# Optimization experiments

Measured on AMD Instinct MI355X. Metric: run time of the kernel, lower is better.

## Reference

```python
import jax, jax.numpy as jnp
import numpy as np

NNZ = 524288
IN_FEATURES = 50000
OUT_FEATURES = 512
N_ROWS = 4096


def setup_inputs() -> dict:
    key = jax.random.key(0)
    k1, k2, k3, k4, k5 = jax.random.split(key, 5)
    values = jax.random.normal(k1, (NNZ,), dtype=jnp.float32)
    weight = jax.random.normal(k2, (IN_FEATURES, OUT_FEATURES), dtype=jnp.float32)
    bias = jax.random.normal(k3, (OUT_FEATURES,), dtype=jnp.float32)
    rows = jax.random.randint(k4, (NNZ,), 0, N_ROWS)
    cols = jax.random.randint(k5, (NNZ,), 0, IN_FEATURES)
    return {
        "values": values,
        "weight": weight,
        "bias": bias,
        "rows": rows,
        "cols": cols,
        "n_rows": N_ROWS,
    }


def reference(values, weight, bias, rows, cols, n_rows):
    # SpMM: out[r, :] = sum_{k: rows[k]==r} values[k] * weight[cols[k], :]
    contrib = values[:, None] * weight[cols]               # [nnz, out]
    out = jax.ops.segment_sum(contrib, rows, num_segments=n_rows)  # [n_rows, out]
    return out + bias
```

## Files before the change

kernel.cpp:

```cpp
#include <hip/hip_runtime.h>
#include <hip/hip_fp16.h>


typedef float f4v __attribute__((ext_vector_type(4)));
typedef int   i4v __attribute__((ext_vector_type(4)));
typedef int   i2v __attribute__((ext_vector_type(2)));

__global__ void convert_count_kernel(const float* __restrict__ weight,
                                     __half* __restrict__ wf16, long long ngroups16,
                                     const int* __restrict__ rows,
                                     int* __restrict__ counts, int nnz) {
    long long i = (long long)blockIdx.x * blockDim.x + threadIdx.x;

    int nquads = nnz >> 2;
    if (i < nquads) {
        i4v r = ((const i4v*)rows)[i];
        atomicAdd(&counts[r.x], 1);
        atomicAdd(&counts[r.y], 1);
        atomicAdd(&counts[r.z], 1);
        atomicAdd(&counts[r.w], 1);
    } else if (i == nquads) {
        for (int k = nquads * 4; k < nnz; ++k) atomicAdd(&counts[rows[k]], 1);
    }

    const f4v* w4 = (const f4v*)weight;
    f4v* dst = (f4v*)wf16;
    long long stride = (long long)gridDim.x * blockDim.x;
    for (long long g = i; g < ngroups16; g += stride) {
        f4v a = w4[4 * g + 0];
        f4v b = w4[4 * g + 1];
        f4v c = w4[4 * g + 2];
        f4v d = w4[4 * g + 3];
        union { __half2 h2[4]; f4v v; } u0, u1;
        u0.h2[0] = __floats2half2_rn(a.x, a.y);
        u0.h2[1] = __floats2half2_rn(a.z, a.w);
        u0.h2[2] = __floats2half2_rn(b.x, b.y);
        u0.h2[3] = __floats2half2_rn(b.z, b.w);
        u1.h2[0] = __floats2half2_rn(c.x, c.y);
        u1.h2[1] = __floats2half2_rn(c.z, c.w);
        u1.h2[2] = __floats2half2_rn(d.x, d.y);
        u1.h2[3] = __floats2half2_rn(d.z, d.w);
        __builtin_nontemporal_store(u0.v, &dst[2 * g]);
        __builtin_nontemporal_store(u1.v, &dst[2 * g + 1]);
    }
}

__global__ void scan_kernel(const int* __restrict__ counts, int* __restrict__ offsets,
                            int* __restrict__ cursor, int n_rows) {
    __shared__ int partial[256];
    const int t = threadIdx.x;
    const int per = (n_rows + 255) / 256;
    const int base = t * per;
    const bool vec = (base + per <= n_rows) && ((per & 3) == 0);

    int sum = 0;
    if (vec) {
        const i4v* c4 = (const i4v*)(counts + base);
        for (int j = 0; j < per / 4; ++j) {
            i4v q = c4[j];
            sum += q.x + q.y + q.z + q.w;
        }
    } else {
        for (int j = 0; j < per; ++j) {
            int idx = base + j;
            if (idx < n_rows) sum += counts[idx];
        }
    }
    partial[t] = sum;
    __syncthreads();
    for (int off = 1; off < 256; off <<= 1) {
        int v = 0;
        if (t >= off) v = partial[t - off];
        __syncthreads();
        if (t >= off) partial[t] += v;
        __syncthreads();
    }
    int run = (t == 0) ? 0 : partial[t - 1];
    if (vec) {
        const i4v* c4 = (const i4v*)(counts + base);
        i4v* o4 = (i4v*)(offsets + base);
        i4v* u4 = (i4v*)(cursor + base);
        for (int j = 0; j < per / 4; ++j) {
            i4v q = c4[j];
            i4v o;
            o.x = run; run += q.x;
            o.y = run; run += q.y;
            o.z = run; run += q.z;
            o.w = run; run += q.w;
            o4[j] = o;
            u4[j] = o;
        }
    } else {
        for (int j = 0; j < per; ++j) {
            int idx = base + j;
            if (idx < n_rows) {
                offsets[idx] = run;
                cursor[idx] = run;
                run += counts[idx];
            }
        }
    }
    if (t == 255) offsets[n_rows] = run;
}

__global__ void scatter_pairs_kernel(const int* __restrict__ rows, const int* __restrict__ cols,
                                     const float* __restrict__ values, int* __restrict__ cursor,
                                     int2* __restrict__ pairs, int nnz) {
    int i = blockIdx.x * blockDim.x + threadIdx.x;
    int nquads = nnz >> 2;
    if (i < nquads) {
        i4v r = ((const i4v*)rows)[i];
        i4v c = ((const i4v*)cols)[i];
        f4v v = ((const f4v*)values)[i];
        int p0 = atomicAdd(&cursor[r.x], 1);
        pairs[p0] = make_int2(c.x, __float_as_int(v.x));
        int p1 = atomicAdd(&cursor[r.y], 1);
        pairs[p1] = make_int2(c.y, __float_as_int(v.y));
        int p2 = atomicAdd(&cursor[r.z], 1);
        pairs[p2] = make_int2(c.z, __float_as_int(v.z));
        int p3 = atomicAdd(&cursor[r.w], 1);
        pairs[p3] = make_int2(c.w, __float_as_int(v.w));
    } else if (i == nquads) {
        for (int k = nquads * 4; k < nnz; ++k) {
            int p = atomicAdd(&cursor[rows[k]], 1);
            pairs[p] = make_int2(cols[k], __float_as_int(values[k]));
        }
    }
}

__global__ __launch_bounds__(256) void accum_f16_kernel(
    const __half* __restrict__ wf16, const float* __restrict__ bias,
    const int* __restrict__ offsets, const int2* __restrict__ pairs,
    float* __restrict__ out, int out_f) {
    const int wave = threadIdx.x >> 6;
    const int lane = threadIdx.x & 63;
    const int row = blockIdx.x;
    const int start = offsets[row];
    const int end = offsets[row + 1];
    const int len = end - start;
    const int per = (len + 3) >> 2;
    int p = start + wave * per;
    int pe = p + per;
    if (pe > end) pe = end;
    if (p > end) p = end;

    const f4v* wbase = (const f4v*)wf16;
    const i2v* pbase = (const i2v*)pairs;
    float acc[8] = {0.f, 0.f, 0.f, 0.f, 0.f, 0.f, 0.f, 0.f};

    for (; p + 4 <= pe; p += 4) {
        i2v e0 = __builtin_nontemporal_load(pbase + p);
        i2v e1 = __builtin_nontemporal_load(pbase + p + 1);
        i2v e2 = __builtin_nontemporal_load(pbase + p + 2);
        i2v e3 = __builtin_nontemporal_load(pbase + p + 3);
        f4v w0 = wbase[(long long)e0.x * 64 + lane];
        f4v w1 = wbase[(long long)e1.x * 64 + lane];
        f4v w2 = wbase[(long long)e2.x * 64 + lane];
        f4v w3 = wbase[(long long)e3.x * 64 + lane];
        float v0 = __int_as_float(e0.y);
        float v1 = __int_as_float(e1.y);
        float v2 = __int_as_float(e2.y);
        float v3 = __int_as_float(e3.y);
        const __half2* h0 = (const __half2*)&w0;
        const __half2* h1 = (const __half2*)&w1;
        const __half2* h2 = (const __half2*)&w2;
        const __half2* h3 = (const __half2*)&w3;
#pragma unroll
        for (int j = 0; j < 4; ++j) {
            float2 f0 = __half22float2(h0[j]);
            float2 f1 = __half22float2(h1[j]);
            float2 f2 = __half22float2(h2[j]);
            float2 f3 = __half22float2(h3[j]);
            acc[2 * j]     += v0 * f0.x + v1 * f1.x + v2 * f2.x + v3 * f3.x;
            acc[2 * j + 1] += v0 * f0.y + v1 * f1.y + v2 * f2.y + v3 * f3.y;
        }
    }
    for (; p < pe; ++p) {
        i2v e0 = __builtin_nontemporal_load(pbase + p);
        float v0 = __int_as_float(e0.y);
        f4v w0 = wbase[(long long)e0.x * 64 + lane];
        const __half2* h0 = (const __half2*)&w0;
#pragma unroll
        for (int j = 0; j < 4; ++j) {
            float2 f0 = __half22float2(h0[j]);
            acc[2 * j]     += v0 * f0.x;
            acc[2 * j + 1] += v0 * f0.y;
        }
    }

    __shared__ float red[4][512];
    {
        float4* dstp = (float4*)&red[wave][lane * 8];
        dstp[0] = make_float4(acc[0], acc[1], acc[2], acc[3]);
        dstp[1] = make_float4(acc[4], acc[5], acc[6], acc[7]);
    }
    __syncthreads();
    const int c = threadIdx.x * 2;
    float s0 = red[0][c] + red[1][c] + red[2][c] + red[3][c];
    float s1 = red[0][c + 1] + red[1][c + 1] + red[2][c + 1] + red[3][c + 1];
    float2 b = *(const float2*)(bias + c);
    *(float2*)(out + (long long)row * out_f + c) = make_float2(s0 + b.x, s1 + b.y);
}

__global__ void count_rows_kernel(const int* __restrict__ rows, int* __restrict__ counts, int nnz) {
    int i = blockIdx.x * blockDim.x + threadIdx.x;
    if (i < nnz) atomicAdd(&counts[rows[i]], 1);
}
__global__ void scatter_kernel(const int* __restrict__ rows, int* __restrict__ cursor,
                               int* __restrict__ perm, int nnz) {
    int i = blockIdx.x * blockDim.x + threadIdx.x;
    if (i < nnz) {
        int p = atomicAdd(&cursor[rows[i]], 1);
        perm[p] = i;
    }
}
__global__ void accum_kernel(const float* __restrict__ values, const float* __restrict__ weight,
                             const float* __restrict__ bias, const int* __restrict__ cols,
                             const int* __restrict__ offsets, const int* __restrict__ perm,
                             float* __restrict__ out, int out_f) {
    const int r = blockIdx.x;
    const int start = offsets[r];
    const int end = offsets[r + 1];
    const int step = blockDim.x * 4;
    for (int base = threadIdx.x * 4; base < out_f; base += step) {
        float4 acc = make_float4(0.f, 0.f, 0.f, 0.f);
        for (int p = start; p < end; ++p) {
            int k = perm[p];
            float v = values[k];
            long long c = cols[k];
            float4 w = *(const float4*)(weight + c * (long long)out_f + base);
            acc.x += v * w.x; acc.y += v * w.y; acc.z += v * w.z; acc.w += v * w.w;
        }
        float4 b = *(const float4*)(bias + base);
        acc.x += b.x; acc.y += b.y; acc.z += b.z; acc.w += b.w;
        *(float4*)(out + (long long)r * out_f + base) = acc;
    }
}

static size_t align_up(size_t x, size_t a) { return (x + a - 1) & ~(a - 1); }

extern "C" void kernel_launch(void* const* d_in, const int* in_sizes, int n_in,
                              void* d_out, int out_size, void* d_ws, size_t ws_size,
                              hipStream_t stream) {
    const float* values = (const float*)d_in[0];
    const float* weight = (const float*)d_in[1];
    const float* bias   = (const float*)d_in[2];
    const int*   rows   = (const int*)d_in[3];
    const int*   cols   = (const int*)d_in[4];

    const int nnz = in_sizes[0];
    const long long wtotal = in_sizes[1];
    const int out_f = in_sizes[2];
    const int n_rows = out_size / out_f;
    float* out = (float*)d_out;

    size_t off_wf16 = 0;
    size_t off_counts = align_up(off_wf16 + (size_t)wtotal * sizeof(__half), 256);
    size_t off_offsets = off_counts + (size_t)n_rows * sizeof(int);
    size_t off_cursor = off_offsets + (size_t)(n_rows + 1) * sizeof(int);
    size_t off_pairs = align_up(off_cursor + (size_t)n_rows * sizeof(int), 256);
    size_t need = off_pairs + (size_t)nnz * sizeof(int2);

    if (ws_size >= need && out_f == 512 && (wtotal % 16) == 0) {
        char* ws = (char*)d_ws;
        __half* wf16 = (__half*)(ws + off_wf16);
        int* counts = (int*)(ws + off_counts);
        int* offsets = (int*)(ws + off_offsets);
        int* cursor = (int*)(ws + off_cursor);
        int2* pairs = (int2*)(ws + off_pairs);

        hipMemsetAsync(counts, 0, (size_t)n_rows * sizeof(int), stream);

        long long ngroups16 = wtotal / 16;
        long long needed = (ngroups16 > (long long)(nnz / 4 + 1)) ? ngroups16
                                                                  : (long long)(nnz / 4 + 1);
        int cc_blocks = (int)((needed + 255) / 256);
        convert_count_kernel<<<cc_blocks, 256, 0, stream>>>(weight, wf16, ngroups16,
                                                            rows, counts, nnz);
        scan_kernel<<<1, 256, 0, stream>>>(counts, offsets, cursor, n_rows);
        int sc_blocks = (nnz / 4 + 1 + 255) / 256;
        scatter_pairs_kernel<<<sc_blocks, 256, 0, stream>>>(rows, cols, values, cursor,
                                                            pairs, nnz);
        accum_f16_kernel<<<n_rows, 256, 0, stream>>>(wf16, bias, offsets, pairs,
                                                     out, out_f);
    } else {
        int* counts = (int*)d_ws;
        int* offsets = counts + n_rows;
        int* cursor = offsets + n_rows + 1;
        int* perm = cursor + n_rows;
        hipMemsetAsync(counts, 0, (size_t)n_rows * sizeof(int), stream);
        int blocks = (nnz + 255) / 256;
        count_rows_kernel<<<blocks, 256, 0, stream>>>(rows, counts, nnz);
        scan_kernel<<<1, 256, 0, stream>>>(counts, offsets, cursor, n_rows);
        scatter_kernel<<<blocks, 256, 0, stream>>>(rows, cursor, perm, nnz);
        accum_kernel<<<n_rows, 128, 0, stream>>>(values, weight, bias, cols,
                                                 offsets, perm, out, out_f);
    }
}
```

Measured before the change: 324.3 us.

## Fuse preprocessing stages into one cooperative kernel with grid-wide syncs

```diff
diff --git a/kernel.cpp b/kernel.cpp
--- a/kernel.cpp
+++ b/kernel.cpp
@@ -1,70 +1,25 @@
 #include <hip/hip_runtime.h>
 #include <hip/hip_fp16.h>
+#include <hip/hip_cooperative_groups.h>
+
+namespace cg = cooperative_groups;
 
 
 typedef float f4v __attribute__((ext_vector_type(4)));
 typedef int   i4v __attribute__((ext_vector_type(4)));
 typedef int   i2v __attribute__((ext_vector_type(2)));
 
-__global__ void convert_count_kernel(const float* __restrict__ weight,
-                                     __half* __restrict__ wf16, long long ngroups16,
-                                     const int* __restrict__ rows,
-                                     int* __restrict__ counts, int nnz) {
-    long long i = (long long)blockIdx.x * blockDim.x + threadIdx.x;
-
-    int nquads = nnz >> 2;
-    if (i < nquads) {
-        i4v r = ((const i4v*)rows)[i];
-        atomicAdd(&counts[r.x], 1);
-        atomicAdd(&counts[r.y], 1);
-        atomicAdd(&counts[r.z], 1);
-        atomicAdd(&counts[r.w], 1);
-    } else if (i == nquads) {
-        for (int k = nquads * 4; k < nnz; ++k) atomicAdd(&counts[rows[k]], 1);
-    }
-
-    const f4v* w4 = (const f4v*)weight;
-    f4v* dst = (f4v*)wf16;
-    long long stride = (long long)gridDim.x * blockDim.x;
-    for (long long g = i; g < ngroups16; g += stride) {
-        f4v a = w4[4 * g + 0];
-        f4v b = w4[4 * g + 1];
-        f4v c = w4[4 * g + 2];
-        f4v d = w4[4 * g + 3];
-        union { __half2 h2[4]; f4v v; } u0, u1;
-        u0.h2[0] = __floats2half2_rn(a.x, a.y);
-        u0.h2[1] = __floats2half2_rn(a.z, a.w);
-        u0.h2[2] = __floats2half2_rn(b.x, b.y);
-        u0.h2[3] = __floats2half2_rn(b.z, b.w);
-        u1.h2[0] = __floats2half2_rn(c.x, c.y);
-        u1.h2[1] = __floats2half2_rn(c.z, c.w);
-        u1.h2[2] = __floats2half2_rn(d.x, d.y);
-        u1.h2[3] = __floats2half2_rn(d.z, d.w);
-        __builtin_nontemporal_store(u0.v, &dst[2 * g]);
-        __builtin_nontemporal_store(u1.v, &dst[2 * g + 1]);
-    }
-}
-
-__global__ void scan_kernel(const int* __restrict__ counts, int* __restrict__ offsets,
-                            int* __restrict__ cursor, int n_rows) {
-    __shared__ int partial[256];
+__device__ inline void scan_block_256(const int* __restrict__ counts,
+                                      int* __restrict__ offsets,
+                                      int* __restrict__ cursor,
+                                      int n_rows, int* partial) {
     const int t = threadIdx.x;
     const int per = (n_rows + 255) / 256;
     const int base = t * per;
-    const bool vec = (base + per <= n_rows) && ((per & 3) == 0);
-
     int sum = 0;
-    if (vec) {
-        const i4v* c4 = (const i4v*)(counts + base);
-        for (int j = 0; j < per / 4; ++j) {
-            i4v q = c4[j];
-            sum += q.x + q.y + q.z + q.w;
-        }
-    } else {
-        for (int j = 0; j < per; ++j) {
-            int idx = base + j;
-            if (idx < n_rows) sum += counts[idx];
-        }
+    for (int j = 0; j < per; ++j) {
+        int idx = base + j;
+        if (idx < n_rows) sum += counts[idx];
     }
     partial[t] = sum;
     __syncthreads();
@@ -76,33 +31,197 @@
         __syncthreads();
     }
     int run = (t == 0) ? 0 : partial[t - 1];
-    if (vec) {
-        const i4v* c4 = (const i4v*)(counts + base);
-        i4v* o4 = (i4v*)(offsets + base);
-        i4v* u4 = (i4v*)(cursor + base);
-        for (int j = 0; j < per / 4; ++j) {
-            i4v q = c4[j];
-            i4v o;
-            o.x = run; run += q.x;
-            o.y = run; run += q.y;
-            o.z = run; run += q.z;
-            o.w = run; run += q.w;
-            o4[j] = o;
-            u4[j] = o;
-        }
-    } else {
-        for (int j = 0; j < per; ++j) {
-            int idx = base + j;
-            if (idx < n_rows) {
-                offsets[idx] = run;
-                cursor[idx] = run;
-                run += counts[idx];
+    for (int j = 0; j < per; ++j) {
+        int idx = base + j;
+        if (idx < n_rows) {
+            offsets[idx] = run;
+            cursor[idx] = run;
+            run += counts[idx];
+        }
+    }
+    if (t == 255) offsets[n_rows] = run;
+}
+
+__global__ __launch_bounds__(256, 8) void prep_kernel(
+    const float* __restrict__ weight, __half* __restrict__ wf16, long long n4,
+    const int* __restrict__ rows, const int* __restrict__ cols,
+    const float* __restrict__ values, int nnz,
+    int* __restrict__ counts, int* __restrict__ offsets,
+    int* __restrict__ cursor, int2* __restrict__ pairs, int n_rows) {
+    __shared__ int partial[256];
+    cg::grid_group grid = cg::this_grid();
+    const long long tid = (long long)blockIdx.x * blockDim.x + threadIdx.x;
+    const long long nth = (long long)gridDim.x * blockDim.x;
+
+    for (long long i = tid; i < n_rows; i += nth) counts[i] = 0;
+    grid.sync();
+
+    {
+        const long long nquads = nnz >> 2;
+        for (long long q = tid; q < nquads; q += nth) {
+            i4v r = ((const i4v*)rows)[q];
+            atomicAdd(&counts[r.x], 1);
+            atomicAdd(&counts[r.y], 1);
+            atomicAdd(&counts[r.z], 1);
+            atomicAdd(&counts[r.w], 1);
+        }
+        if (tid == 0)
+            for (int k = (int)(nquads << 2); k < nnz; ++k) atomicAdd(&counts[rows[k]], 1);
+
+        const f4v* __restrict__ w4 = (const f4v*)weight;
+        i2v* __restrict__ dst = (i2v*)wf16;
+        long long g = tid;
+        for (; g + nth < n4; g += 2 * nth) {
+            f4v a = w4[g];
+            f4v b = w4[g + nth];
+            union { __half2 h2[2]; i2v v; } ua, ub;
+            ua.h2[0] = __floats2half2_rn(a.x, a.y);
+            ua.h2[1] = __floats2half2_rn(a.z, a.w);
+            ub.h2[0] = __floats2half2_rn(b.x, b.y);
+            ub.h2[1] = __floats2half2_rn(b.z, b.w);
+            dst[g] = ua.v;
+            dst[g + nth] = ub.v;
+        }
+        for (; g < n4; g += nth) {
+            f4v a = w4[g];
+            union { __half2 h2[2]; i2v v; } ua;
+            ua.h2[0] = __floats2half2_rn(a.x, a.y);
+            ua.h2[1] = __floats2half2_rn(a.z, a.w);
+            dst[g] = ua.v;
+        }
+    }
+    grid.sync();
+
+    if (blockIdx.x == 0) scan_block_256(counts, offsets, cursor, n_rows, partial);
+    grid.sync();
+
+    {
+        const long long nquads = nnz >> 2;
+        for (long long q = tid; q < nquads; q += nth) {
+            i4v r = ((const i4v*)rows)[q];
+            i4v c = ((const i4v*)cols)[q];
+            f4v v = ((const f4v*)values)[q];
+            int p0 = atomicAdd(&cursor[r.x], 1);
+            pairs[p0] = make_int2(c.x, __float_as_int(v.x));
+            int p1 = atomicAdd(&cursor[r.y], 1);
+            pairs[p1] = make_int2(c.y, __float_as_int(v.y));
+            int p2 = atomicAdd(&cursor[r.z], 1);
+            pairs[p2] = make_int2(c.z, __float_as_int(v.z));
+            int p3 = atomicAdd(&cursor[r.w], 1);
+            pairs[p3] = make_int2(c.w, __float_as_int(v.w));
+        }
+        if (tid == 0)
+            for (int k = (int)(nquads << 2); k < nnz; ++k) {
+                int p = atomicAdd(&cursor[rows[k]], 1);
+                pairs[p] = make_int2(cols[k], __float_as_int(values[k]));
             }
-        }
-    }
-    if (t == 255) offsets[n_rows] = run;
-}
-
+    }
+}
+
+__global__ __launch_bounds__(256) void accum_f16_kernel(
+    const __half* __restrict__ wf16, const float* __restrict__ bias,
+    const int* __restrict__ offsets, const int2* __restrict__ pairs,
+    float* __restrict__ out, int out_f) {
+    const int wave = threadIdx.x >> 6;
+    const int lane = threadIdx.x & 63;
+    const int row = blockIdx.x;
+    const int start = offsets[row];
+    const int end = offsets[row + 1];
+    const int len = end - start;
+    const int per = (len + 3) >> 2;
+    int p = start + wave * per;
+    int pe = p + per;
+    if (pe > end) pe = end;
+    if (p > end) p = end;
+
+    const f4v* wbase = (const f4v*)wf16;
+    float acc[8] = {0.f, 0.f, 0.f, 0.f, 0.f, 0.f, 0.f, 0.f};
+
+    for (; p + 4 <= pe; p += 4) {
+        int2 e0 = pairs[p];
+        int2 e1 = pairs[p + 1];
+        int2 e2 = pairs[p + 2];
+        int2 e3 = pairs[p + 3];
+        f4v w0 = wbase[(long long)e0.x * 64 + lane];
+        f4v w1 = wbase[(long long)e1.x * 64 + lane];
+        f4v w2 = wbase[(long long)e2.x * 64 + lane];
+        f4v w3 = wbase[(long long)e3.x * 64 + lane];
+        float v0 = __int_as_float(e0.y);
+        float v1 = __int_as_float(e1.y);
+        float v2 = __int_as_float(e2.y);
+        float v3 = __int_as_float(e3.y);
+        const __half2* h0 = (const __half2*)&w0;
+        const __half2* h1 = (const __half2*)&w1;
+        const __half2* h2 = (const __half2*)&w2;
+        const __half2* h3 = (const __half2*)&w3;
+#pragma unroll
+        for (int j = 0; j < 4; ++j) {
+            float2 f0 = __half22float2(h0[j]);
+            float2 f1 = __half22float2(h1[j]);
+            float2 f2 = __half22float2(h2[j]);
+            float2 f3 = __half22float2(h3[j]);
+            acc[2 * j]     += v0 * f0.x + v1 * f1.x + v2 * f2.x + v3 * f3.x;
+            acc[2 * j + 1] += v0 * f0.y + v1 * f1.y + v2 * f2.y + v3 * f3.y;
+        }
+    }
+    for (; p < pe; ++p) {
+        int2 e0 = pairs[p];
+        float v0 = __int_as_float(e0.y);
+        f4v w0 = wbase[(long long)e0.x * 64 + lane];
+        const __half2* h0 = (const __half2*)&w0;
+#pragma unroll
+        for (int j = 0; j < 4; ++j) {
+            float2 f0 = __half22float2(h0[j]);
+            acc[2 * j]     += v0 * f0.x;
+            acc[2 * j + 1] += v0 * f0.y;
+        }
+    }
+
+    __shared__ float red[4][512];
+    {
+        float4* dstp = (float4*)&red[wave][lane * 8];
+        dstp[0] = make_float4(acc[0], acc[1], acc[2], acc[3]);
+        dstp[1] = make_float4(acc[4], acc[5], acc[6], acc[7]);
+    }
+    __syncthreads();
+    const int c = threadIdx.x * 2;
+    float s0 = red[0][c] + red[1][c] + red[2][c] + red[3][c];
+    float s1 = red[0][c + 1] + red[1][c + 1] + red[2][c + 1] + red[3][c + 1];
+    float2 b = *(const float2*)(bias + c);
+    *(float2*)(out + (long long)row * out_f + c) = make_float2(s0 + b.x, s1 + b.y);
+}
+
+__global__ void convert_count_kernel(const float* __restrict__ weight,
+                                     __half* __restrict__ wf16, long long n4,
+                                     const int* __restrict__ rows,
+                                     int* __restrict__ counts, int nnz) {
+    long long i = (long long)blockIdx.x * blockDim.x + threadIdx.x;
+    long long nth = (long long)gridDim.x * blockDim.x;
+    long long nquads = nnz >> 2;
+    for (long long q = i; q < nquads; q += nth) {
+        i4v r = ((const i4v*)rows)[q];
+        atomicAdd(&counts[r.x], 1);
+        atomicAdd(&counts[r.y], 1);
+        atomicAdd(&counts[r.z], 1);
+        atomicAdd(&counts[r.w], 1);
+    }
+    if (i == 0)
+        for (int k = (int)(nquads << 2); k < nnz; ++k) atomicAdd(&counts[rows[k]], 1);
+    const f4v* w4 = (const f4v*)weight;
+    i2v* dst = (i2v*)wf16;
+    for (long long g = i; g < n4; g += nth) {
+        f4v a = w4[g];
+        union { __half2 h2[2]; i2v v; } ua;
+        ua.h2[0] = __floats2half2_rn(a.x, a.y);
+        ua.h2[1] = __floats2half2_rn(a.z, a.w);
+        dst[g] = ua.v;
+    }
+}
+__global__ void scan_kernel(const int* __restrict__ counts, int* __restrict__ offsets,
+                            int* __restrict__ cursor, int n_rows) {
+    __shared__ int partial[256];
+    scan_block_256(counts, offsets, cursor, n_rows, partial);
+}
 __global__ void scatter_pairs_kernel(const int* __restrict__ rows, const int* __restrict__ cols,
                                      const float* __restrict__ values, int* __restrict__ cursor,
                                      int2* __restrict__ pairs, int nnz) {
@@ -128,80 +247,6 @@
     }
 }
 
-__global__ __launch_bounds__(256) void accum_f16_kernel(
-    const __half* __restrict__ wf16, const float* __restrict__ bias,
-    const int* __restrict__ offsets, const int2* __restrict__ pairs,
-    float* __restrict__ out, int out_f) {
-    const int wave = threadIdx.x >> 6;
-    const int lane = threadIdx.x & 63;
-    const int row = blockIdx.x;
-    const int start = offsets[row];
-    const int end = offsets[row + 1];
-    const int len = end - start;
-    const int per = (len + 3) >> 2;
-    int p = start + wave * per;
-    int pe = p + per;
-    if (pe > end) pe = end;
-    if (p > end) p = end;
-
-    const f4v* wbase = (const f4v*)wf16;
-    const i2v* pbase = (const i2v*)pairs;
-    float acc[8] = {0.f, 0.f, 0.f, 0.f, 0.f, 0.f, 0.f, 0.f};
-
-    for (; p + 4 <= pe; p += 4) {
-        i2v e0 = __builtin_nontemporal_load(pbase + p);
-        i2v e1 = __builtin_nontemporal_load(pbase + p + 1);
-        i2v e2 = __builtin_nontemporal_load(pbase + p + 2);
-        i2v e3 = __builtin_nontemporal_load(pbase + p + 3);
-        f4v w0 = wbase[(long long)e0.x * 64 + lane];
-        f4v w1 = wbase[(long long)e1.x * 64 + lane];
-        f4v w2 = wbase[(long long)e2.x * 64 + lane];
-        f4v w3 = wbase[(long long)e3.x * 64 + lane];
-        float v0 = __int_as_float(e0.y);
-        float v1 = __int_as_float(e1.y);
-        float v2 = __int_as_float(e2.y);
-        float v3 = __int_as_float(e3.y);
-        const __half2* h0 = (const __half2*)&w0;
-        const __half2* h1 = (const __half2*)&w1;
-        const __half2* h2 = (const __half2*)&w2;
-        const __half2* h3 = (const __half2*)&w3;
-#pragma unroll
-        for (int j = 0; j < 4; ++j) {
-            float2 f0 = __half22float2(h0[j]);
-            float2 f1 = __half22float2(h1[j]);
-            float2 f2 = __half22float2(h2[j]);
-            float2 f3 = __half22float2(h3[j]);
-            acc[2 * j]     += v0 * f0.x + v1 * f1.x + v2 * f2.x + v3 * f3.x;
-            acc[2 * j + 1] += v0 * f0.y + v1 * f1.y + v2 * f2.y + v3 * f3.y;
-        }
-    }
-    for (; p < pe; ++p) {
-        i2v e0 = __builtin_nontemporal_load(pbase + p);
-        float v0 = __int_as_float(e0.y);
-        f4v w0 = wbase[(long long)e0.x * 64 + lane];
-        const __half2* h0 = (const __half2*)&w0;
-#pragma unroll
-        for (int j = 0; j < 4; ++j) {
-            float2 f0 = __half22float2(h0[j]);
-            acc[2 * j]     += v0 * f0.x;
-            acc[2 * j + 1] += v0 * f0.y;
-        }
-    }
-
-    __shared__ float red[4][512];
-    {
-        float4* dstp = (float4*)&red[wave][lane * 8];
-        dstp[0] = make_float4(acc[0], acc[1], acc[2], acc[3]);
-        dstp[1] = make_float4(acc[4], acc[5], acc[6], acc[7]);
-    }
-    __syncthreads();
-    const int c = threadIdx.x * 2;
-    float s0 = red[0][c] + red[1][c] + red[2][c] + red[3][c];
-    float s1 = red[0][c + 1] + red[1][c + 1] + red[2][c + 1] + red[3][c + 1];
-    float2 b = *(const float2*)(bias + c);
-    *(float2*)(out + (long long)row * out_f + c) = make_float2(s0 + b.x, s1 + b.y);
-}
-
 __global__ void count_rows_kernel(const int* __restrict__ rows, int* __restrict__ counts, int nnz) {
     int i = blockIdx.x * blockDim.x + threadIdx.x;
     if (i < nnz) atomicAdd(&counts[rows[i]], 1);
@@ -261,26 +306,56 @@
     size_t off_pairs = align_up(off_cursor + (size_t)n_rows * sizeof(int), 256);
     size_t need = off_pairs + (size_t)nnz * sizeof(int2);
 
-    if (ws_size >= need && out_f == 512 && (wtotal % 16) == 0) {
+    if (ws_size >= need && out_f == 512 && (wtotal % 4) == 0) {
         char* ws = (char*)d_ws;
         __half* wf16 = (__half*)(ws + off_wf16);
         int* counts = (int*)(ws + off_counts);
         int* offsets = (int*)(ws + off_offsets);
         int* cursor = (int*)(ws + off_cursor);
         int2* pairs = (int2*)(ws + off_pairs);
-
-        hipMemsetAsync(counts, 0, (size_t)n_rows * sizeof(int), stream);
-
-        long long ngroups16 = wtotal / 16;
-        long long needed = (ngroups16 > (long long)(nnz / 4 + 1)) ? ngroups16
-                                                                  : (long long)(nnz / 4 + 1);
-        int cc_blocks = (int)((needed + 255) / 256);
-        convert_count_kernel<<<cc_blocks, 256, 0, stream>>>(weight, wf16, ngroups16,
-                                                            rows, counts, nnz);
-        scan_kernel<<<1, 256, 0, stream>>>(counts, offsets, cursor, n_rows);
-        int sc_blocks = (nnz / 4 + 1 + 255) / 256;
-        scatter_pairs_kernel<<<sc_blocks, 256, 0, stream>>>(rows, cols, values, cursor,
-                                                            pairs, nnz);
+        long long n4 = wtotal / 4;
+
+        static int coop_grid = 0;
+        if (coop_grid == 0) {
+            int g = 1024;
+            int maxb = 0;
+            if (hipOccupancyMaxActiveBlocksPerMultiprocessor(
+                    &maxb, (const void*)prep_kernel, 256, 0) == hipSuccess && maxb > 0) {
+                long long cap = (long long)maxb * 256 ;
+                if (cap < g) g = (int)cap;
+                if (cap > 2048) cap = 2048;
+                g = (int)cap;
+            }
+            coop_grid = g;
+        }
+
+        const float* a_weight = weight;
+        __half* a_wf16 = wf16;
+        long long a_n4 = n4;
+        const int* a_rows = rows;
+        const int* a_cols = cols;
+        const float* a_values = values;
+        int a_nnz = nnz;
+        int* a_counts = counts;
+        int* a_offsets = offsets;
+        int* a_cursor = cursor;
+        int2* a_pairs = pairs;
+        int a_nrows = n_rows;
+        void* args[] = {&a_weight, &a_wf16, &a_n4, &a_rows, &a_cols, &a_values,
+                        &a_nnz, &a_counts, &a_offsets, &a_cursor, &a_pairs, &a_nrows};
+
+        hipError_t e = hipLaunchCooperativeKernel((const void*)prep_kernel,
+                                                  dim3(coop_grid), dim3(256),
+                                                  args, 0, stream);
+        if (e != hipSuccess) {
+            hipMemsetAsync(counts, 0, (size_t)n_rows * sizeof(int), stream);
+            convert_count_kernel<<<2048, 256, 0, stream>>>(weight, wf16, n4, rows,
+                                                           counts, nnz);
+            scan_kernel<<<1, 256, 0, stream>>>(counts, offsets, cursor, n_rows);
+            int sc_blocks = (nnz / 4 + 1 + 255) / 256;
+            scatter_pairs_kernel<<<sc_blocks, 256, 0, stream>>>(rows, cols, values,
+                                                                cursor, pairs, nnz);
+        }
         accum_f16_kernel<<<n_rows, 256, 0, stream>>>(wf16, bias, offsets, pairs,
                                                      out, out_f);
     } else {
```

Result: slower. 833.8 us (+157.1%).

## Use fixed-capacity per-row buckets and fuse scatter with weight conversion

Applied to the files above, without the earlier changes.

```diff
diff --git a/kernel.cpp b/kernel.cpp
--- a/kernel.cpp
+++ b/kernel.cpp
@@ -4,67 +4,171 @@
 
 typedef float f4v __attribute__((ext_vector_type(4)));
 typedef int   i4v __attribute__((ext_vector_type(4)));
-typedef int   i2v __attribute__((ext_vector_type(2)));
+
+__global__ __launch_bounds__(256) void scatter_convert_kernel(
+    const float* __restrict__ weight, __half* __restrict__ wf16, long long ngroups8,
+    const int* __restrict__ rows, const int* __restrict__ cols,
+    const float* __restrict__ values, int nnz,
+    int* __restrict__ cnt, int2* __restrict__ pairs, int cap) {
+    const long long tid = (long long)blockIdx.x * blockDim.x + threadIdx.x;
+    const long long nth = (long long)gridDim.x * blockDim.x;
+
+    const long long nquads = nnz >> 2;
+    for (long long q = tid; q < nquads; q += nth) {
+        i4v r = ((const i4v*)rows)[q];
+        i4v c = ((const i4v*)cols)[q];
+        f4v v = ((const f4v*)values)[q];
+        int p0 = atomicAdd(&cnt[r.x], 1);
+        if (p0 < cap) pairs[(long long)r.x * cap + p0] = make_int2(c.x, __float_as_int(v.x));
+        int p1 = atomicAdd(&cnt[r.y], 1);
+        if (p1 < cap) pairs[(long long)r.y * cap + p1] = make_int2(c.y, __float_as_int(v.y));
+        int p2 = atomicAdd(&cnt[r.z], 1);
+        if (p2 < cap) pairs[(long long)r.z * cap + p2] = make_int2(c.z, __float_as_int(v.z));
+        int p3 = atomicAdd(&cnt[r.w], 1);
+        if (p3 < cap) pairs[(long long)r.w * cap + p3] = make_int2(c.w, __float_as_int(v.w));
+    }
+    if (tid == 0) {
+        for (int k = (int)(nquads << 2); k < nnz; ++k) {
+            int p = atomicAdd(&cnt[rows[k]], 1);
+            if (p < cap) pairs[(long long)rows[k] * cap + p] = make_int2(cols[k], __float_as_int(values[k]));
+        }
+    }
+
+    const f4v* __restrict__ w4 = (const f4v*)weight;
+    f4v* __restrict__ dst = (f4v*)wf16;
+    for (long long g = tid; g < ngroups8; g += nth) {
+        f4v a = w4[2 * g];
+        f4v b = w4[2 * g + 1];
+        union { __half2 h2[4]; f4v v; } u;
+        u.h2[0] = __floats2half2_rn(a.x, a.y);
+        u.h2[1] = __floats2half2_rn(a.z, a.w);
+        u.h2[2] = __floats2half2_rn(b.x, b.y);
+        u.h2[3] = __floats2half2_rn(b.z, b.w);
+        dst[g] = u.v;
+    }
+}
+
+__global__ __launch_bounds__(256) void accum_f16_kernel(
+    const __half* __restrict__ wf16, const float* __restrict__ bias,
+    const int* __restrict__ meta, const int2* __restrict__ pairs,
+    float* __restrict__ out, int out_f, int cap) {
+    const int wave = threadIdx.x >> 6;
+    const int lane = threadIdx.x & 63;
+    const int row = blockIdx.x;
+    long long base;
+    int len;
+    if (cap > 0) {
+        base = (long long)row * cap;
+        len = meta[row];
+        if (len > cap) len = cap;
+    } else {
+        int s = meta[row];
+        base = s;
+        len = meta[row + 1] - s;
+    }
+    const int per = (len + 3) >> 2;
+    int p = wave * per;
+    int pe = p + per;
+    if (pe > len) pe = len;
+    if (p > len) p = len;
+
+    const f4v* wbase = (const f4v*)wf16;
+    const int2* prow = pairs + base;
+    float acc[8] = {0.f, 0.f, 0.f, 0.f, 0.f, 0.f, 0.f, 0.f};
+
+    for (; p + 4 <= pe; p += 4) {
+        int2 e0 = prow[p];
+        int2 e1 = prow[p + 1];
+        int2 e2 = prow[p + 2];
+        int2 e3 = prow[p + 3];
+        f4v w0 = wbase[(long long)e0.x * 64 + lane];
+        f4v w1 = wbase[(long long)e1.x * 64 + lane];
+        f4v w2 = wbase[(long long)e2.x * 64 + lane];
+        f4v w3 = wbase[(long long)e3.x * 64 + lane];
+        float v0 = __int_as_float(e0.y);
+        float v1 = __int_as_float(e1.y);
+        float v2 = __int_as_float(e2.y);
+        float v3 = __int_as_float(e3.y);
+        const __half2* h0 = (const __half2*)&w0;
+        const __half2* h1 = (const __half2*)&w1;
+        const __half2* h2 = (const __half2*)&w2;
+        const __half2* h3 = (const __half2*)&w3;
+#pragma unroll
+        for (int j = 0; j < 4; ++j) {
+            float2 f0 = __half22float2(h0[j]);
+            float2 f1 = __half22float2(h1[j]);
+            float2 f2 = __half22float2(h2[j]);
+            float2 f3 = __half22float2(h3[j]);
+            acc[2 * j]     += v0 * f0.x + v1 * f1.x + v2 * f2.x + v3 * f3.x;
+            acc[2 * j + 1] += v0 * f0.y + v1 * f1.y + v2 * f2.y + v3 * f3.y;
+        }
+    }
+    for (; p < pe; ++p) {
+        int2 e0 = prow[p];
+        float v0 = __int_as_float(e0.y);
+        f4v w0 = wbase[(long long)e0.x * 64 + lane];
+        const __half2* h0 = (const __half2*)&w0;
+#pragma unroll
+        for (int j = 0; j < 4; ++j) {
+            float2 f0 = __half22float2(h0[j]);
+            acc[2 * j]     += v0 * f0.x;
+            acc[2 * j + 1] += v0 * f0.y;
+        }
+    }
+
+    __shared__ float red[4][512];
+    {
+        float4* dstp = (float4*)&red[wave][lane * 8];
+        dstp[0] = make_float4(acc[0], acc[1], acc[2], acc[3]);
+        dstp[1] = make_float4(acc[4], acc[5], acc[6], acc[7]);
+    }
+    __syncthreads();
+    const int c = threadIdx.x * 2;
+    float s0 = red[0][c] + red[1][c] + red[2][c] + red[3][c];
+    float s1 = red[0][c + 1] + red[1][c + 1] + red[2][c + 1] + red[3][c + 1];
+    float2 b = *(const float2*)(bias + c);
+    *(float2*)(out + (long long)row * out_f + c) = make_float2(s0 + b.x, s1 + b.y);
+}
 
 __global__ void convert_count_kernel(const float* __restrict__ weight,
-                                     __half* __restrict__ wf16, long long ngroups16,
+                                     __half* __restrict__ wf16, long long ngroups8,
                                      const int* __restrict__ rows,
                                      int* __restrict__ counts, int nnz) {
     long long i = (long long)blockIdx.x * blockDim.x + threadIdx.x;
-
-    int nquads = nnz >> 2;
-    if (i < nquads) {
-        i4v r = ((const i4v*)rows)[i];
+    long long nth = (long long)gridDim.x * blockDim.x;
+    long long nquads = nnz >> 2;
+    for (long long q = i; q < nquads; q += nth) {
+        i4v r = ((const i4v*)rows)[q];
         atomicAdd(&counts[r.x], 1);
         atomicAdd(&counts[r.y], 1);
         atomicAdd(&counts[r.z], 1);
         atomicAdd(&counts[r.w], 1);
-    } else if (i == nquads) {
-        for (int k = nquads * 4; k < nnz; ++k) atomicAdd(&counts[rows[k]], 1);
-    }
-
+    }
+    if (i == 0)
+        for (int k = (int)(nquads << 2); k < nnz; ++k) atomicAdd(&counts[rows[k]], 1);
     const f4v* w4 = (const f4v*)weight;
     f4v* dst = (f4v*)wf16;
-    long long stride = (long long)gridDim.x * blockDim.x;
-    for (long long g = i; g < ngroups16; g += stride) {
-        f4v a = w4[4 * g + 0];
-        f4v b = w4[4 * g + 1];
-        f4v c = w4[4 * g + 2];
-        f4v d = w4[4 * g + 3];
-        union { __half2 h2[4]; f4v v; } u0, u1;
-        u0.h2[0] = __floats2half2_rn(a.x, a.y);
-        u0.h2[1] = __floats2half2_rn(a.z, a.w);
-        u0.h2[2] = __floats2half2_rn(b.x, b.y);
-        u0.h2[3] = __floats2half2_rn(b.z, b.w);
-        u1.h2[0] = __floats2half2_rn(c.x, c.y);
-        u1.h2[1] = __floats2half2_rn(c.z, c.w);
-        u1.h2[2] = __floats2half2_rn(d.x, d.y);
-        u1.h2[3] = __floats2half2_rn(d.z, d.w);
-        __builtin_nontemporal_store(u0.v, &dst[2 * g]);
-        __builtin_nontemporal_store(u1.v, &dst[2 * g + 1]);
-    }
-}
-
+    for (long long g = i; g < ngroups8; g += nth) {
+        f4v a = w4[2 * g];
+        f4v b = w4[2 * g + 1];
+        union { __half2 h2[4]; f4v v; } u;
+        u.h2[0] = __floats2half2_rn(a.x, a.y);
+        u.h2[1] = __floats2half2_rn(a.z, a.w);
+        u.h2[2] = __floats2half2_rn(b.x, b.y);
+        u.h2[3] = __floats2half2_rn(b.z, b.w);
+        dst[g] = u.v;
+    }
+}
 __global__ void scan_kernel(const int* __restrict__ counts, int* __restrict__ offsets,
                             int* __restrict__ cursor, int n_rows) {
     __shared__ int partial[256];
     const int t = threadIdx.x;
     const int per = (n_rows + 255) / 256;
     const int base = t * per;
-    const bool vec = (base + per <= n_rows) && ((per & 3) == 0);
-
     int sum = 0;
-    if (vec) {
-        const i4v* c4 = (const i4v*)(counts + base);
-        for (int j = 0; j < per / 4; ++j) {
-            i4v q = c4[j];
-            sum += q.x + q.y + q.z + q.w;
-        }
-    } else {
-        for (int j = 0; j < per; ++j) {
-            int idx = base + j;
-            if (idx < n_rows) sum += counts[idx];
-        }
+    for (int j = 0; j < per; ++j) {
+        int idx = base + j;
+        if (idx < n_rows) sum += counts[idx];
     }
     partial[t] = sum;
     __syncthreads();
@@ -76,33 +180,16 @@
         __syncthreads();
     }
     int run = (t == 0) ? 0 : partial[t - 1];
-    if (vec) {
-        const i4v* c4 = (const i4v*)(counts + base);
-        i4v* o4 = (i4v*)(offsets + base);
-        i4v* u4 = (i4v*)(cursor + base);
-        for (int j = 0; j < per / 4; ++j) {
-            i4v q = c4[j];
-            i4v o;
-            o.x = run; run += q.x;
-            o.y = run; run += q.y;
-            o.z = run; run += q.z;
-            o.w = run; run += q.w;
-            o4[j] = o;
-            u4[j] = o;
-        }
-    } else {
-        for (int j = 0; j < per; ++j) {
-            int idx = base + j;
-            if (idx < n_rows) {
-                offsets[idx] = run;
-                cursor[idx] = run;
-                run += counts[idx];
-            }
+    for (int j = 0; j < per; ++j) {
+        int idx = base + j;
+        if (idx < n_rows) {
+            offsets[idx] = run;
+            cursor[idx] = run;
+            run += counts[idx];
         }
     }
     if (t == 255) offsets[n_rows] = run;
 }
-
 __global__ void scatter_pairs_kernel(const int* __restrict__ rows, const int* __restrict__ cols,
                                      const float* __restrict__ values, int* __restrict__ cursor,
                                      int2* __restrict__ pairs, int nnz) {
@@ -128,80 +215,6 @@
     }
 }
 
-__global__ __launch_bounds__(256) void accum_f16_kernel(
-    const __half* __restrict__ wf16, const float* __restrict__ bias,
-    const int* __restrict__ offsets, const int2* __restrict__ pairs,
-    float* __restrict__ out, int out_f) {
-    const int wave = threadIdx.x >> 6;
-    const int lane = threadIdx.x & 63;
-    const int row = blockIdx.x;
-    const int start = offsets[row];
-    const int end = offsets[row + 1];
-    const int len = end - start;
-    const int per = (len + 3) >> 2;
-    int p = start + wave * per;
-    int pe = p + per;
-    if (pe > end) pe = end;
-    if (p > end) p = end;
-
-    const f4v* wbase = (const f4v*)wf16;
-    const i2v* pbase = (const i2v*)pairs;
-    float acc[8] = {0.f, 0.f, 0.f, 0.f, 0.f, 0.f, 0.f, 0.f};
-
-    for (; p + 4 <= pe; p += 4) {
-        i2v e0 = __builtin_nontemporal_load(pbase + p);
-        i2v e1 = __builtin_nontemporal_load(pbase + p + 1);
-        i2v e2 = __builtin_nontemporal_load(pbase + p + 2);
-        i2v e3 = __builtin_nontemporal_load(pbase + p + 3);
-        f4v w0 = wbase[(long long)e0.x * 64 + lane];
-        f4v w1 = wbase[(long long)e1.x * 64 + lane];
-        f4v w2 = wbase[(long long)e2.x * 64 + lane];
-        f4v w3 = wbase[(long long)e3.x * 64 + lane];
-        float v0 = __int_as_float(e0.y);
-        float v1 = __int_as_float(e1.y);
-        float v2 = __int_as_float(e2.y);
-        float v3 = __int_as_float(e3.y);
-        const __half2* h0 = (const __half2*)&w0;
-        const __half2* h1 = (const __half2*)&w1;
-        const __half2* h2 = (const __half2*)&w2;
-        const __half2* h3 = (const __half2*)&w3;
-#pragma unroll
-        for (int j = 0; j < 4; ++j) {
-            float2 f0 = __half22float2(h0[j]);
-            float2 f1 = __half22float2(h1[j]);
-            float2 f2 = __half22float2(h2[j]);
-            float2 f3 = __half22float2(h3[j]);
-            acc[2 * j]     += v0 * f0.x + v1 * f1.x + v2 * f2.x + v3 * f3.x;
-            acc[2 * j + 1] += v0 * f0.y + v1 * f1.y + v2 * f2.y + v3 * f3.y;
-        }
-    }
-    for (; p < pe; ++p) {
-        i2v e0 = __builtin_nontemporal_load(pbase + p);
-        float v0 = __int_as_float(e0.y);
-        f4v w0 = wbase[(long long)e0.x * 64 + lane];
-        const __half2* h0 = (const __half2*)&w0;
-#pragma unroll
-        for (int j = 0; j < 4; ++j) {
-            float2 f0 = __half22float2(h0[j]);
-            acc[2 * j]     += v0 * f0.x;
-            acc[2 * j + 1] += v0 * f0.y;
-        }
-    }
-
-    __shared__ float red[4][512];
-    {
-        float4* dstp = (float4*)&red[wave][lane * 8];
-        dstp[0] = make_float4(acc[0], acc[1], acc[2], acc[3]);
-        dstp[1] = make_float4(acc[4], acc[5], acc[6], acc[7]);
-    }
-    __syncthreads();
-    const int c = threadIdx.x * 2;
-    float s0 = red[0][c] + red[1][c] + red[2][c] + red[3][c];
-    float s1 = red[0][c + 1] + red[1][c + 1] + red[2][c + 1] + red[3][c + 1];
-    float2 b = *(const float2*)(bias + c);
-    *(float2*)(out + (long long)row * out_f + c) = make_float2(s0 + b.x, s1 + b.y);
-}
-
 __global__ void count_rows_kernel(const int* __restrict__ rows, int* __restrict__ counts, int nnz) {
     int i = blockIdx.x * blockDim.x + threadIdx.x;
     if (i < nnz) atomicAdd(&counts[rows[i]], 1);
@@ -254,36 +267,64 @@
     const int n_rows = out_size / out_f;
     float* out = (float*)d_out;
 
-    size_t off_wf16 = 0;
-    size_t off_counts = align_up(off_wf16 + (size_t)wtotal * sizeof(__half), 256);
+    const bool shape_ok = (out_f == 512) && ((wtotal % 8) == 0) && (n_rows > 0);
+
+    size_t off_cnt = align_up((size_t)wtotal * sizeof(__half), 256);
+    size_t off_pairs_slots = align_up(off_cnt + (size_t)n_rows * sizeof(int), 256);
+    int cap = 0;
+    if (shape_ok && ws_size > off_pairs_slots) {
+        size_t slack = (ws_size - off_pairs_slots) / ((size_t)n_rows * sizeof(int2));
+        cap = (int)(slack > 512 ? 512 : slack);
+        int mean = (n_rows > 0) ? nnz / n_rows : 0;
+        if (cap < mean + 96) cap = 0;
+    }
+
+    if (cap > 0) {
+        char* ws = (char*)d_ws;
+        __half* wf16 = (__half*)ws;
+        int* cnt = (int*)(ws + off_cnt);
+        int2* pairs = (int2*)(ws + off_pairs_slots);
+        long long ngroups8 = wtotal / 8;
+
+        hipMemsetAsync(cnt, 0, (size_t)n_rows * sizeof(int), stream);
+        scatter_convert_kernel<<<2048, 256, 0, stream>>>(weight, wf16, ngroups8,
+                                                         rows, cols, values, nnz,
+                                                         cnt, pairs, cap);
+        accum_f16_kernel<<<n_rows, 256, 0, stream>>>(wf16, bias, cnt, pairs,
+                                                     out, out_f, cap);
+        return;
+    }
+
+    size_t off_counts = align_up((size_t)wtotal * sizeof(__half), 256);
     size_t off_offsets = off_counts + (size_t)n_rows * sizeof(int);
     size_t off_cursor = off_offsets + (size_t)(n_rows + 1) * sizeof(int);
     size_t off_pairs = align_up(off_cursor + (size_t)n_rows * sizeof(int), 256);
     size_t need = off_pairs + (size_t)nnz * sizeof(int2);
 
-    if (ws_size >= need && out_f == 512 && (wtotal % 16) == 0) {
+    if (shape_ok && ws_size >= need) {
         char* ws = (char*)d_ws;
-        __half* wf16 = (__half*)(ws + off_wf16);
+        __half* wf16 = (__half*)ws;
         int* counts = (int*)(ws + off_counts);
         int* offsets = (int*)(ws + off_offsets);
         int* cursor = (int*)(ws + off_cursor);
         int2* pairs = (int2*)(ws + off_pairs);
+        long long ngroups8 = wtotal / 8;
 
         hipMemsetAsync(counts, 0, (size_t)n_rows * sizeof(int), stream);
-
-        long long ngroups16 = wtotal / 16;
-        long long needed = (ngroups16 > (long long)(nnz / 4 + 1)) ? ngroups16
-                                                                  : (long long)(nnz / 4 + 1);
-        int cc_blocks = (int)((needed + 255) / 256);
-        convert_count_kernel<<<cc_blocks, 256, 0, stream>>>(weight, wf16, ngroups16,
+        int cc_blocks = (int)((ngroups8 + 255) / 256);
+        if (cc_blocks > 12800) cc_blocks = 12800;
+        convert_count_kernel<<<cc_blocks, 256, 0, stream>>>(weight, wf16, ngroups8,
                                                             rows, counts, nnz);
         scan_kernel<<<1, 256, 0, stream>>>(counts, offsets, cursor, n_rows);
         int sc_blocks = (nnz / 4 + 1 + 255) / 256;
-        scatter_pairs_kernel<<<sc_blocks, 256, 0, stream>>>(rows, cols, values, cursor,
-                                                            pairs, nnz);
+        scatter_pairs_kernel<<<sc_blocks, 256, 0, stream>>>(rows, cols, values,
+                                                            cursor, pairs, nnz);
         accum_f16_kernel<<<n_rows, 256, 0, stream>>>(wf16, bias, offsets, pairs,
-                                                     out, out_f);
-    } else {
+                                                     out, out_f, 0);
+        return;
+    }
+
+    {
         int* counts = (int*)d_ws;
         int* offsets = counts + n_rows;
         int* cursor = offsets + n_rows + 1;
```

Result: faster. 276.0 us (-14.9%).
